# Performance work log

Measured on AMD Instinct MI355X. Metric: run time of the kernel, lower is better.

## Reference

```python
import jax, jax.numpy as jnp
import numpy as np
from jax.ops import segment_sum

N_GRAPHS, N_PER = 100, 1000
N = N_GRAPHS * N_PER
DEG = 32
E = N * DEG
RATIO = 0.8
K = int(np.ceil(RATIO * N_PER))  # 800, equal-size graphs -> fixed k
F_IN, F_MID, F_OUT = 128, 16, 256


def setup_inputs() -> dict:
    key = jax.random.key(0)
    ks = jax.random.split(key, 10)
    x = jax.random.normal(ks[0], (N, F_IN), dtype=jnp.float32)
    # intra-graph random edges
    epg = E // N_GRAPHS
    src_l = jax.random.randint(ks[1], (N_GRAPHS, epg), 0, N_PER)
    dst_l = jax.random.randint(ks[2], (N_GRAPHS, epg), 0, N_PER)
    offs = (jnp.arange(N_GRAPHS) * N_PER)[:, None]
    edge_index = jnp.stack([(src_l + offs).reshape(-1), (dst_l + offs).reshape(-1)]).astype(jnp.int32)
    batch = jnp.repeat(jnp.arange(N_GRAPHS, dtype=jnp.int32), N_PER)
    s = lambda fan: 1.0 / np.sqrt(fan)
    W1 = jax.random.normal(ks[3], (F_IN, F_MID), dtype=jnp.float32) * s(F_IN)
    b1 = jnp.zeros((F_MID,), dtype=jnp.float32)
    w_rel = jax.random.normal(ks[4], (F_MID, 1), dtype=jnp.float32) * s(F_MID)
    b_rel = jnp.zeros((1,), dtype=jnp.float32)
    w_root = jax.random.normal(ks[5], (F_MID, 1), dtype=jnp.float32) * s(F_MID)
    W2 = jax.random.normal(ks[6], (F_MID, F_OUT), dtype=jnp.float32) * s(F_MID)
    b2 = jnp.zeros((F_OUT,), dtype=jnp.float32)
    return {"x": x, "edge_index": edge_index, "batch": batch,
            "W1": W1, "b1": b1, "w_rel": w_rel, "b_rel": b_rel,
            "w_root": w_root, "W2": W2, "b2": b2}


def _gcn(x, src, dst, W, b, self_w, ew, n):
    # GCNConv with self-loops: D^{-1/2}(A+I)D^{-1/2} X W + b; masked variant
    deg = segment_sum(ew, dst, num_segments=n) + self_w
    dis = jnp.where(deg > 0, jax.lax.rsqrt(deg), 0.0)
    xw = x @ W
    coef = ew * dis[src] * dis[dst]                       # [E]
    agg = segment_sum(xw[src] * coef[:, None], dst, num_segments=n)
    agg = agg + xw * (self_w * dis * dis)[:, None]        # self-loop term
    return agg + b


def reference(x, edge_index, batch, W1, b1, w_rel, b_rel, w_root, W2, b2):
    src, dst = edge_index[0], edge_index[1]
    ones_n = jnp.ones((N,), dtype=x.dtype)
    ones_e = jnp.ones((src.shape[0],), dtype=x.dtype)
    # conv1 + relu
    h = jax.nn.relu(_gcn(x, src, dst, W1, b1, ones_n, ones_e, N))
    # SAGPooling score: GraphConv(16,1) -> tanh
    agg = segment_sum(h[src], dst, num_segments=N)
    score = jnp.tanh((agg @ w_rel + h @ w_root + b_rel)[:, 0])  # [N]
    # per-graph top-k (equal graph sizes -> fixed K), expressed as node mask
    sc2 = score.reshape(N_GRAPHS, N_PER)
    _, idx = jax.lax.top_k(sc2, K)
    mask = jnp.zeros((N_GRAPHS, N_PER), dtype=x.dtype)
    mask = mask.at[jnp.arange(N_GRAPHS)[:, None], idx].set(1.0).reshape(-1)  # [N]
    h = h * (score * mask)[:, None]                       # x[perm] * score[perm]
    em = mask[src] * mask[dst]                            # filter_adj as edge mask
    # conv2 + relu on surviving nodes only
    h2 = jax.nn.relu(_gcn(h, src, dst, W2, b2, mask, em, N)) * mask[:, None]
    # global mean pool over surviving nodes per graph
    sums = segment_sum(h2, batch, num_segments=N_GRAPHS)
    cnt = segment_sum(mask, batch, num_segments=N_GRAPHS)
    return sums / cnt[:, None]
```

## Files before the change

### kernel.cpp

```cpp
#include <hip/hip_runtime.h>
#include <math.h>

#define N_NODES 100000
#define NG 100
#define N_PER 1000
#define N_EDGES 3200000
#define EPG 32000
#define EPG4 8000
#define EPGP 35008
#define K_TOP 800
#define F_IN 128
#define F_MID 16
#define F_OUT 256
#define SENT 1000
#define NCH 8
#define CHN 128

typedef __attribute__((ext_vector_type(8))) short short8;
typedef __attribute__((ext_vector_type(4))) float floatx4;

__device__ __forceinline__ unsigned short f2bf(float x) {
    union { float f; unsigned int u; } c; c.f = x;
    unsigned int u = c.u;
    u = u + 0x7FFF + ((u >> 16) & 1);
    return (unsigned short)(u >> 16);
}
__device__ __forceinline__ void add4(float4& a, const float4 b) {
    a.x += b.x; a.y += b.y; a.z += b.z; a.w += b.w;
}
__device__ __forceinline__ unsigned int fkey(float f) {
    unsigned int u = __float_as_uint(f);
    return (u & 0x80000000u) ? ~u : (u | 0x80000000u);
}

__global__ __launch_bounds__(1024) void k_front(const float* __restrict__ x,
    const float* __restrict__ W1, const int* __restrict__ ei,
    unsigned short* __restrict__ csr, int* __restrict__ crG,
    float* __restrict__ dis1G, float* __restrict__ xw1)
{
    __shared__ int cnts[N_PER];
    __shared__ int rs[N_PER];
    __shared__ int scan[1024];
    __shared__ unsigned int rank4[EPG4];
    __shared__ __align__(16) unsigned short csrl[EPGP];

    int b = blockIdx.x, t = threadIdx.x;
    if (b < NG) {
        int g = b, ebase = g * EPG, nbase = g * N_PER;
        if (b == 0 && t < F_MID) xw1[(size_t)N_NODES * F_MID + t] = 0.f;
        const int4* dst4 = (const int4*)(ei + N_EDGES + ebase);
        const int4* src4 = (const int4*)(ei + ebase);
        if (t < N_PER) cnts[t] = 0;
        __syncthreads();
        for (int i = t; i < EPG4; i += 1024) {
            int4 d = dst4[i];
            unsigned r0 = (unsigned)atomicAdd(&cnts[d.x - nbase], 1);
            unsigned r1 = (unsigned)atomicAdd(&cnts[d.y - nbase], 1);
            unsigned r2 = (unsigned)atomicAdd(&cnts[d.z - nbase], 1);
            unsigned r3 = (unsigned)atomicAdd(&cnts[d.w - nbase], 1);
            rank4[i] = r0 | (r1 << 8) | (r2 << 16) | (r3 << 24);
        }
        __syncthreads();
        int c = (t < N_PER) ? cnts[t] : 0;
        int c4 = (c + 3) & ~3;
        scan[t] = c4;
        __syncthreads();
        for (int dd = 1; dd < 1024; dd <<= 1) {
            int v = (t >= dd) ? scan[t - dd] : 0;
            __syncthreads();
            scan[t] += v;
            __syncthreads();
        }
        int exc = scan[t] - c4;
        if (t < N_PER) {
            rs[t] = exc;
            crG[nbase + t] = (c << 16) | exc;
            dis1G[nbase + t] = rsqrtf((float)c + 1.0f);
            for (int q = c; q < c4; q++) csrl[exc + q] = (unsigned short)SENT;
        }
        __syncthreads();
        for (int i = t; i < EPG4; i += 1024) {
            int4 d = dst4[i];
            int4 s = src4[i];
            unsigned rk = rank4[i];
            csrl[rs[d.x - nbase] + (rk & 255u)]         = (unsigned short)(s.x - nbase);
            csrl[rs[d.y - nbase] + ((rk >> 8) & 255u)]  = (unsigned short)(s.y - nbase);
            csrl[rs[d.z - nbase] + ((rk >> 16) & 255u)] = (unsigned short)(s.z - nbase);
            csrl[rs[d.w - nbase] + (rk >> 24)]          = (unsigned short)(s.w - nbase);
        }
        __syncthreads();
        {
            const uint4* sv = (const uint4*)csrl;
            uint4* dv = (uint4*)(csr + (size_t)g * EPGP);
            for (int i = t; i < EPGP / 8; i += 1024) dv[i] = sv[i];
        }
    } else {
        int n = (b - NG) * 1024 + t;
        if (n >= N_NODES) return;
        const float4* xr = (const float4*)(x + (size_t)n * F_IN);
        float4 a0 = {0,0,0,0}, a1 = a0, a2 = a0, a3 = a0;
#pragma unroll 4
        for (int kk = 0; kk < 32; kk++) {
            float4 xv = xr[kk];
#pragma unroll
            for (int r = 0; r < 4; r++) {
                const float4* wr = (const float4*)(W1 + (kk * 4 + r) * F_MID);
                float xs = (r == 0) ? xv.x : (r == 1) ? xv.y : (r == 2) ? xv.z : xv.w;
                float4 w0 = wr[0], w1 = wr[1], w2 = wr[2], w3 = wr[3];
                a0.x = fmaf(xs, w0.x, a0.x); a0.y = fmaf(xs, w0.y, a0.y);
                a0.z = fmaf(xs, w0.z, a0.z); a0.w = fmaf(xs, w0.w, a0.w);
                a1.x = fmaf(xs, w1.x, a1.x); a1.y = fmaf(xs, w1.y, a1.y);
                a1.z = fmaf(xs, w1.z, a1.z); a1.w = fmaf(xs, w1.w, a1.w);
                a2.x = fmaf(xs, w2.x, a2.x); a2.y = fmaf(xs, w2.y, a2.y);
                a2.z = fmaf(xs, w2.z, a2.z); a2.w = fmaf(xs, w2.w, a2.w);
                a3.x = fmaf(xs, w3.x, a3.x); a3.y = fmaf(xs, w3.y, a3.y);
                a3.z = fmaf(xs, w3.z, a3.z); a3.w = fmaf(xs, w3.w, a3.w);
            }
        }
        float4* op = (float4*)(xw1 + (size_t)n * F_MID);
        op[0] = a0; op[1] = a1; op[2] = a2; op[3] = a3;
    }
}

__global__ __launch_bounds__(512) void k_conv1(const unsigned short* __restrict__ csr,
    const int* __restrict__ crG,
    const float* __restrict__ dis1G, const float* __restrict__ xw1,
    const float* __restrict__ b1, const float* __restrict__ w_rel,
    const float* __restrict__ w_root,
    float* __restrict__ hG, float* __restrict__ hwG, float* __restrict__ hroG)
{
    __shared__ float dis1l[N_PER + 1];
    int t = threadIdx.x, b = blockIdx.x;
    int g = b % NG, chunk = b / NG;
    int nbase = g * N_PER;
    const unsigned short* cg = csr + (size_t)g * EPGP;
    if (b == 0 && t < F_MID) hG[(size_t)N_NODES * F_MID + t] = 0.f;
    for (int i = t; i < N_PER; i += 512) dis1l[i] = dis1G[nbase + i];
    if (t == 0) dis1l[SENT] = 0.f;
    __syncthreads();

    int grp = t >> 2, l = t & 3;
    int n = chunk * CHN + grp;
    if (n >= N_PER) return;
    int cr = crG[nbase + n];
    int c4 = ((cr >> 16) + 3) & ~3;
    const unsigned short* cp = cg + (cr & 0xFFFF);
    float4 a0 = {0,0,0,0}, a1 = a0, a2 = a0, a3 = a0;
    for (int k = 0; k < c4; k += 4) {
        uint2 wv = *(const uint2*)(cp + k);
        int s0 = wv.x & 0xFFFF, s1 = wv.x >> 16, s2 = wv.y & 0xFFFF, s3 = wv.y >> 16;
        float4 v0 = *(const float4*)(xw1 + ((size_t)(nbase + s0) << 4) + 4 * l);
        float4 v1 = *(const float4*)(xw1 + ((size_t)(nbase + s1) << 4) + 4 * l);
        float4 v2 = *(const float4*)(xw1 + ((size_t)(nbase + s2) << 4) + 4 * l);
        float4 v3 = *(const float4*)(xw1 + ((size_t)(nbase + s3) << 4) + 4 * l);
        float w0 = dis1l[s0], w1 = dis1l[s1], w2 = dis1l[s2], w3 = dis1l[s3];
        a0.x = fmaf(v0.x, w0, a0.x); a0.y = fmaf(v0.y, w0, a0.y); a0.z = fmaf(v0.z, w0, a0.z); a0.w = fmaf(v0.w, w0, a0.w);
        a1.x = fmaf(v1.x, w1, a1.x); a1.y = fmaf(v1.y, w1, a1.y); a1.z = fmaf(v1.z, w1, a1.z); a1.w = fmaf(v1.w, w1, a1.w);
        a2.x = fmaf(v2.x, w2, a2.x); a2.y = fmaf(v2.y, w2, a2.y); a2.z = fmaf(v2.z, w2, a2.z); a2.w = fmaf(v2.w, w2, a2.w);
        a3.x = fmaf(v3.x, w3, a3.x); a3.y = fmaf(v3.y, w3, a3.y); a3.z = fmaf(v3.z, w3, a3.z); a3.w = fmaf(v3.w, w3, a3.w);
    }
    add4(a0, a1); add4(a2, a3); add4(a0, a2);
    float dn = dis1l[n];
    float4 sfr = *(const float4*)(xw1 + ((size_t)(nbase + n) << 4) + 4 * l);
    float4 b14 = *(const float4*)(b1 + 4 * l);
    float4 hv;
    hv.x = fmaxf(fmaf(dn, fmaf(sfr.x, dn, a0.x), b14.x), 0.f);
    hv.y = fmaxf(fmaf(dn, fmaf(sfr.y, dn, a0.y), b14.y), 0.f);
    hv.z = fmaxf(fmaf(dn, fmaf(sfr.z, dn, a0.z), b14.z), 0.f);
    hv.w = fmaxf(fmaf(dn, fmaf(sfr.w, dn, a0.w), b14.w), 0.f);
    *(float4*)(hG + ((size_t)(nbase + n) << 4) + 4 * l) = hv;

    float4 wr4 = *(const float4*)(w_rel + 4 * l);
    float4 wo4 = *(const float4*)(w_root + 4 * l);
    float p1 = hv.x * wr4.x + hv.y * wr4.y + hv.z * wr4.z + hv.w * wr4.w;
    float p2 = hv.x * wo4.x + hv.y * wo4.y + hv.z * wo4.z + hv.w * wo4.w;
    p1 += __shfl_xor(p1, 1); p1 += __shfl_xor(p1, 2);
    p2 += __shfl_xor(p2, 1); p2 += __shfl_xor(p2, 2);
    if (l == 0) { hwG[nbase + n] = p1; hroG[nbase + n] = p2; }
}

__global__ __launch_bounds__(1024) void k_mid(const unsigned short* __restrict__ csr,
    const int* __restrict__ crG,
    const float* __restrict__ hwG, const float* __restrict__ hroG,
    const float* __restrict__ b_rel,
    float* __restrict__ mskG, float* __restrict__ dis2G, float* __restrict__ wsrcG,
    float* __restrict__ out)
{
    __shared__ float hwl[N_PER + 1];
    __shared__ float sc[N_PER];
    __shared__ float msk[N_PER + 1];
    __shared__ int cntl[N_PER];
    __shared__ int rsl[N_PER];
    __shared__ int hist[1024];
    __shared__ int sh_b1, sh_r1, sh_b2, sh_r2, sh_len, sh_cntgt;
    __shared__ float sh_thr;

    int t = threadIdx.x, g = blockIdx.x;
    int nbase = g * N_PER;
    const unsigned short* cg = csr + (size_t)g * EPGP;
    int grp = t >> 2, l = t & 3;

    if (t < N_PER) {
        int cr = crG[nbase + t];
        cntl[t] = cr >> 16; rsl[t] = cr & 0xFFFF;
        hwl[t] = hwG[nbase + t];
    }
    if (t == 0) { sh_cntgt = 0; sh_len = 0; hwl[SENT] = 0.f; }
    if (t < F_OUT) out[g * F_OUT + t] = 0.f;
    float brel = b_rel[0];
    __syncthreads();

#pragma unroll
    for (int rr = 0; rr < 4; rr++) {
        int n = grp + 256 * rr;
        if (n < N_PER) {
            int c4 = (cntl[n] + 3) & ~3;
            const unsigned short* cp = cg + rsl[n];
            float sm = 0.f;
            for (int k = 0; k < c4; k += 4) {
                uint2 wv = *(const uint2*)(cp + k);
                int s = (l == 0) ? (int)(wv.x & 0xFFFF) : (l == 1) ? (int)(wv.x >> 16)
                      : (l == 2) ? (int)(wv.y & 0xFFFF) : (int)(wv.y >> 16);
                sm += hwl[s];
            }
            sm += __shfl_xor(sm, 1); sm += __shfl_xor(sm, 2);
            if (l == 0) sc[n] = tanhf(sm + hroG[nbase + n] + brel);
        }
    }
    __syncthreads();

    unsigned int mykey = (t < N_PER) ? fkey(sc[t]) : 0u;
    hist[t] = 0;
    __syncthreads();
    if (t < N_PER) atomicAdd(&hist[mykey >> 22], 1);
    __syncthreads();
    {
        int v0 = hist[t]; __syncthreads();
        hist[1023 - t] = v0; __syncthreads();
        for (int dd = 1; dd < 1024; dd <<= 1) {
            int v = (t >= dd) ? hist[t - dd] : 0;
            __syncthreads(); hist[t] += v; __syncthreads();
        }
        int Sb = hist[1023 - t];
        int Snext = (t == 1023) ? 0 : hist[1022 - t];
        if (Sb >= K_TOP && Snext < K_TOP) { sh_b1 = t; sh_r1 = K_TOP - Snext; }
    }
    __syncthreads();
    int b1v = sh_b1, r1 = sh_r1;
    hist[t] = 0;
    __syncthreads();
    if (t < N_PER && (int)(mykey >> 22) == b1v) atomicAdd(&hist[(mykey >> 12) & 1023], 1);
    __syncthreads();
    {
        int v0 = hist[t]; __syncthreads();
        hist[1023 - t] = v0; __syncthreads();
        for (int dd = 1; dd < 1024; dd <<= 1) {
            int v = (t >= dd) ? hist[t - dd] : 0;
            __syncthreads(); hist[t] += v; __syncthreads();
        }
        int Sb = hist[1023 - t];
        int Snext = (t == 1023) ? 0 : hist[1022 - t];
        if (Sb >= r1 && Snext < r1) { sh_b2 = t; sh_r2 = r1 - Snext; }
    }
    __syncthreads();
    unsigned int pref = ((unsigned int)b1v << 10) | (unsigned int)sh_b2;
    int r2 = sh_r2;
    __syncthreads();
    if (t < N_PER && (mykey >> 12) == pref) { int p = atomicAdd(&sh_len, 1); hist[p] = (int)mykey; }
    __syncthreads();
    {
        int L = sh_len;
        if (t < L) {
            unsigned int k0 = (unsigned int)hist[t];
            int gcnt = 0, ecnt = 0;
            for (int q2 = 0; q2 < L; q2++) {
                unsigned int kq = (unsigned int)hist[q2];
                gcnt += (kq > k0); ecnt += (kq == k0);
            }
            if (gcnt < r2 && r2 <= gcnt + ecnt)
                sh_thr = __uint_as_float((k0 & 0x80000000u) ? (k0 & 0x7FFFFFFFu) : ~k0);
        }
    }
    __syncthreads();
    float thr = sh_thr;

    {
        bool pred = (t < N_PER) && (sc[t] > thr);
        unsigned long long bal = __ballot(pred);
        if ((t & 63) == 0) atomicAdd(&sh_cntgt, (int)__popcll(bal));
    }
    __syncthreads();
    {
        int need = K_TOP - sh_cntgt;
        if (t < N_PER) {
            float v = sc[t];
            float mm;
            if (v > thr) mm = 1.f;
            else if (v < thr) mm = 0.f;
            else {
                int r = 0;
                for (int q2 = 0; q2 < t; q2++) if (sc[q2] == thr) r++;
                mm = (r < need) ? 1.f : 0.f;
            }
            msk[t] = mm;
        }
        if (t == 0) msk[SENT] = 0.f;
    }
    __syncthreads();

#pragma unroll
    for (int rr = 0; rr < 4; rr++) {
        int n = grp + 256 * rr;
        if (n < N_PER) {
            int c4 = (cntl[n] + 3) & ~3;
            const unsigned short* cp = cg + rsl[n];
            float sm = 0.f;
            for (int k = 0; k < c4; k += 4) {
                uint2 wv = *(const uint2*)(cp + k);
                int s = (l == 0) ? (int)(wv.x & 0xFFFF) : (l == 1) ? (int)(wv.x >> 16)
                      : (l == 2) ? (int)(wv.y & 0xFFFF) : (int)(wv.y >> 16);
                sm += msk[s];
            }
            sm += __shfl_xor(sm, 1); sm += __shfl_xor(sm, 2);
            if (l == 0) {
                float d2 = msk[n] * (sm + 1.f);
                float di = (d2 > 0.f) ? rsqrtf(d2) : 0.f;
                mskG[nbase + n] = msk[n];
                dis2G[nbase + n] = di;
                wsrcG[nbase + n] = sc[n] * msk[n] * di;
            }
        }
    }
}

__global__ __launch_bounds__(512) void k_conv2(const unsigned short* __restrict__ csr,
    const int* __restrict__ crG,
    const float* __restrict__ hG, const float* __restrict__ wsrcG,
    const float* __restrict__ dis2G, const float* __restrict__ mskG,
    const float* __restrict__ W2, const float* __restrict__ b2,
    float* __restrict__ out)
{
    __shared__ float wsrcl[N_PER + 1];
    __shared__ __align__(16) unsigned short fbf[CHN * F_MID];
    __shared__ __align__(16) unsigned short w2t[F_OUT * F_MID];
    __shared__ float mskl[CHN];
    int t = threadIdx.x, b = blockIdx.x;
    int g = b % NG, chunk = b / NG;
    int nbase = g * N_PER, n0 = chunk * CHN;
    const unsigned short* cg = csr + (size_t)g * EPGP;

    for (int i = t; i < N_PER; i += 512) wsrcl[i] = wsrcG[nbase + i];
    if (t == 0) wsrcl[SENT] = 0.f;
    for (int i = t; i < F_OUT * F_MID; i += 512) {
        int f = i >> 4, jj = i & 15;
        w2t[i] = f2bf(W2[jj * F_OUT + f]);
    }
    __syncthreads();

    int grp = t >> 2, l = t & 3;
    int n = n0 + grp;
    if (n < N_PER) {
        float di = dis2G[nbase + n];
        float4 pv = {0.f, 0.f, 0.f, 0.f};
        if (di != 0.f) {
            int cr = crG[nbase + n];
            int c4 = ((cr >> 16) + 3) & ~3;
            const unsigned short* cp = cg + (cr & 0xFFFF);
            float4 a0 = {0,0,0,0}, a1 = a0, a2 = a0, a3 = a0;
            for (int k = 0; k < c4; k += 4) {
                uint2 wv = *(const uint2*)(cp + k);
                int s0 = wv.x & 0xFFFF, s1 = wv.x >> 16, s2 = wv.y & 0xFFFF, s3 = wv.y >> 16;
                float4 v0 = *(const float4*)(hG + ((size_t)(nbase + s0) << 4) + 4 * l);
                float4 v1 = *(const float4*)(hG + ((size_t)(nbase + s1) << 4) + 4 * l);
                float4 v2 = *(const float4*)(hG + ((size_t)(nbase + s2) << 4) + 4 * l);
                float4 v3 = *(const float4*)(hG + ((size_t)(nbase + s3) << 4) + 4 * l);
                float w0 = wsrcl[s0], w1 = wsrcl[s1], w2 = wsrcl[s2], w3 = wsrcl[s3];
                a0.x = fmaf(v0.x, w0, a0.x); a0.y = fmaf(v0.y, w0, a0.y); a0.z = fmaf(v0.z, w0, a0.z); a0.w = fmaf(v0.w, w0, a0.w);
                a1.x = fmaf(v1.x, w1, a1.x); a1.y = fmaf(v1.y, w1, a1.y); a1.z = fmaf(v1.z, w1, a1.z); a1.w = fmaf(v1.w, w1, a1.w);
                a2.x = fmaf(v2.x, w2, a2.x); a2.y = fmaf(v2.y, w2, a2.y); a2.z = fmaf(v2.z, w2, a2.z); a2.w = fmaf(v2.w, w2, a2.w);
                a3.x = fmaf(v3.x, w3, a3.x); a3.y = fmaf(v3.y, w3, a3.y); a3.z = fmaf(v3.z, w3, a3.z); a3.w = fmaf(v3.w, w3, a3.w);
            }
            add4(a0, a1); add4(a2, a3); add4(a0, a2);
            float wn = wsrcl[n];
            float4 hs = *(const float4*)(hG + ((size_t)(nbase + n) << 4) + 4 * l);
            pv.x = di * fmaf(hs.x, wn, a0.x);
            pv.y = di * fmaf(hs.y, wn, a0.y);
            pv.z = di * fmaf(hs.z, wn, a0.z);
            pv.w = di * fmaf(hs.w, wn, a0.w);
        }
        unsigned int pk0 = (unsigned int)f2bf(pv.x) | ((unsigned int)f2bf(pv.y) << 16);
        unsigned int pk1 = (unsigned int)f2bf(pv.z) | ((unsigned int)f2bf(pv.w) << 16);
        *(unsigned int*)(fbf + grp * F_MID + 4 * l) = pk0;
        *(unsigned int*)(fbf + grp * F_MID + 4 * l + 2) = pk1;
        if (l == 0) mskl[grp] = mskG[nbase + n];
    } else {
        *(unsigned int*)(fbf + grp * F_MID + 4 * l) = 0u;
        *(unsigned int*)(fbf + grp * F_MID + 4 * l + 2) = 0u;
        if (l == 0) mskl[grp] = 0.f;
    }
    __syncthreads();

    {
        int wave = t >> 6, lane = t & 63;
        int q = lane >> 4, fl = lane & 15;
        int c0 = 32 * wave + fl, c1 = c0 + 16;
        float b2f0 = b2[c0], b2f1 = b2[c1];
        short8 bfrag0 = {0,0,0,0,0,0,0,0}, bfrag1 = bfrag0;
        if (q < 2) {
            bfrag0 = *(const short8*)(w2t + c0 * F_MID + q * 8);
            bfrag1 = *(const short8*)(w2t + c1 * F_MID + q * 8);
        }
        floatx4 zero = {0.f, 0.f, 0.f, 0.f};
        float acc0 = 0.f, acc1 = 0.f;
        for (int tile = 0; tile < CHN / 16; tile++) {
            short8 afrag = {0,0,0,0,0,0,0,0};
            int na = tile * 16 + fl;
            if (q < 2)
                afrag = *(const short8*)(fbf + na * F_MID + q * 8);
            floatx4 d0 = __builtin_amdgcn_mfma_f32_16x16x32_bf16(afrag, bfrag0, zero, 0, 0, 0);
            floatx4 d1 = __builtin_amdgcn_mfma_f32_16x16x32_bf16(afrag, bfrag1, zero, 0, 0, 0);
#pragma unroll
            for (int r = 0; r < 4; r++) {
                int nd = tile * 16 + q * 4 + r;
                float m = mskl[nd];
                acc0 += m * fmaxf(d0[r] + b2f0, 0.f);
                acc1 += m * fmaxf(d1[r] + b2f1, 0.f);
            }
        }
        acc0 += __shfl_xor(acc0, 16); acc0 += __shfl_xor(acc0, 32);
        acc1 += __shfl_xor(acc1, 16); acc1 += __shfl_xor(acc1, 32);
        if (lane < 16) {
            atomicAdd(&out[g * F_OUT + c0], acc0 * (1.0f / (float)K_TOP));
            atomicAdd(&out[g * F_OUT + c1], acc1 * (1.0f / (float)K_TOP));
        }
    }
}

extern "C" void kernel_launch(void* const* d_in, const int* in_sizes, int n_in,
                              void* d_out, int out_size, void* d_ws, size_t ws_size,
                              hipStream_t stream) {
    const float* x      = (const float*)d_in[0];
    const int*   ei     = (const int*)d_in[1];
    const float* W1     = (const float*)d_in[3];
    const float* b1     = (const float*)d_in[4];
    const float* w_rel  = (const float*)d_in[5];
    const float* b_rel  = (const float*)d_in[6];
    const float* w_root = (const float*)d_in[7];
    const float* W2     = (const float*)d_in[8];
    const float* b2     = (const float*)d_in[9];
    float* out = (float*)d_out;

    char* ws = (char*)d_ws;
    size_t o = 0;
    auto nxt = [&](size_t bytes) { void* p = ws + o; o += (bytes + 255) & ~(size_t)255; return p; };
    unsigned short* csr = (unsigned short*)nxt((size_t)NG * EPGP * sizeof(unsigned short));
    int*   crG   = (int*)nxt((size_t)N_NODES * sizeof(int));
    float* dis1G = (float*)nxt((size_t)N_NODES * sizeof(float));
    float* xw1   = (float*)nxt(((size_t)N_NODES + 1) * F_MID * sizeof(float));
    float* hG    = (float*)nxt(((size_t)N_NODES + 1) * F_MID * sizeof(float));
    float* hwG   = (float*)nxt((size_t)N_NODES * sizeof(float));
    float* hroG  = (float*)nxt((size_t)N_NODES * sizeof(float));
    float* mskG  = (float*)nxt((size_t)N_NODES * sizeof(float));
    float* dis2G = (float*)nxt((size_t)N_NODES * sizeof(float));
    float* wsrcG = (float*)nxt((size_t)N_NODES * sizeof(float));

    int gemm_blocks = (N_NODES + 1023) / 1024;
    k_front<<<NG + gemm_blocks, 1024, 0, stream>>>(x, W1, ei, csr, crG, dis1G, xw1);
    k_conv1<<<NG * NCH, 512, 0, stream>>>(csr, crG, dis1G, xw1, b1, w_rel, w_root, hG, hwG, hroG);
    k_mid<<<NG, 1024, 0, stream>>>(csr, crG, hwG, hroG, b_rel, mskG, dis2G, wsrcG, out);
    k_conv2<<<NG * NCH, 512, 0, stream>>>(csr, crG, hG, wsrcG, dis2G, mskG, W2, b2, out);
}
```

Before: 224.7 us.

## Stage pre-scaled per-graph features in LDS for conv gathers

Both GCN aggregation kernels now copy the whole graph's feature rows into shared memory, pre-multiplied by the per-source normalisation weight. The neighbour gathers then become plain adds from swizzled LDS instead of scattered global loads plus multiplies. The swizzle is meant to reduce bank conflicts. In exchange, each block loads the full graph even though it only processes one chunk of nodes, and the large LDS footprint may cut occupancy. The global sentinel-row zeroing is also dropped.

```diff
diff --git a/kernel.cpp b/kernel.cpp
--- a/kernel.cpp
+++ b/kernel.cpp
@@ -27,6 +27,9 @@
 }
 __device__ __forceinline__ void add4(float4& a, const float4 b) {
     a.x += b.x; a.y += b.y; a.z += b.z; a.w += b.w;
+}
+__device__ __forceinline__ int fidx4(int s, int l) {
+    return s * 16 + ((4 * (l + ((s >> 1) & 3))) & 15);
 }
 __device__ __forceinline__ unsigned int fkey(float f) {
     unsigned int u = __float_as_uint(f);
@@ -129,14 +132,22 @@
     const float* __restrict__ w_root,
     float* __restrict__ hG, float* __restrict__ hwG, float* __restrict__ hroG)
 {
-    __shared__ float dis1l[N_PER + 1];
+    __shared__ __align__(16) float feat[(N_PER + 1) * F_MID];
     int t = threadIdx.x, b = blockIdx.x;
     int g = b % NG, chunk = b / NG;
     int nbase = g * N_PER;
     const unsigned short* cg = csr + (size_t)g * EPGP;
-    if (b == 0 && t < F_MID) hG[(size_t)N_NODES * F_MID + t] = 0.f;
-    for (int i = t; i < N_PER; i += 512) dis1l[i] = dis1G[nbase + i];
-    if (t == 0) dis1l[SENT] = 0.f;
+    {
+        const float4* xsrc = (const float4*)(xw1 + (size_t)nbase * F_MID);
+        for (int i = t; i < N_PER * 4; i += 512) {
+            int nn = i >> 2, q = i & 3;
+            float4 v = xsrc[i];
+            float d = dis1G[nbase + nn];
+            v.x *= d; v.y *= d; v.z *= d; v.w *= d;
+            *(float4*)(feat + fidx4(nn, q)) = v;
+        }
+        if (t < 4) { float4 z = {0.f, 0.f, 0.f, 0.f}; *(float4*)(feat + fidx4(SENT, t)) = z; }
+    }
     __syncthreads();
 
     int grp = t >> 2, l = t & 3;
@@ -149,25 +160,20 @@
     for (int k = 0; k < c4; k += 4) {
         uint2 wv = *(const uint2*)(cp + k);
         int s0 = wv.x & 0xFFFF, s1 = wv.x >> 16, s2 = wv.y & 0xFFFF, s3 = wv.y >> 16;
-        float4 v0 = *(const float4*)(xw1 + ((size_t)(nbase + s0) << 4) + 4 * l);
-        float4 v1 = *(const float4*)(xw1 + ((size_t)(nbase + s1) << 4) + 4 * l);
-        float4 v2 = *(const float4*)(xw1 + ((size_t)(nbase + s2) << 4) + 4 * l);
-        float4 v3 = *(const float4*)(xw1 + ((size_t)(nbase + s3) << 4) + 4 * l);
-        float w0 = dis1l[s0], w1 = dis1l[s1], w2 = dis1l[s2], w3 = dis1l[s3];
-        a0.x = fmaf(v0.x, w0, a0.x); a0.y = fmaf(v0.y, w0, a0.y); a0.z = fmaf(v0.z, w0, a0.z); a0.w = fmaf(v0.w, w0, a0.w);
-        a1.x = fmaf(v1.x, w1, a1.x); a1.y = fmaf(v1.y, w1, a1.y); a1.z = fmaf(v1.z, w1, a1.z); a1.w = fmaf(v1.w, w1, a1.w);
-        a2.x = fmaf(v2.x, w2, a2.x); a2.y = fmaf(v2.y, w2, a2.y); a2.z = fmaf(v2.z, w2, a2.z); a2.w = fmaf(v2.w, w2, a2.w);
-        a3.x = fmaf(v3.x, w3, a3.x); a3.y = fmaf(v3.y, w3, a3.y); a3.z = fmaf(v3.z, w3, a3.z); a3.w = fmaf(v3.w, w3, a3.w);
+        add4(a0, *(const float4*)(feat + fidx4(s0, l)));
+        add4(a1, *(const float4*)(feat + fidx4(s1, l)));
+        add4(a2, *(const float4*)(feat + fidx4(s2, l)));
+        add4(a3, *(const float4*)(feat + fidx4(s3, l)));
     }
     add4(a0, a1); add4(a2, a3); add4(a0, a2);
-    float dn = dis1l[n];
-    float4 sfr = *(const float4*)(xw1 + ((size_t)(nbase + n) << 4) + 4 * l);
+    float dn = dis1G[nbase + n];
+    float4 sf = *(const float4*)(feat + fidx4(n, l));
     float4 b14 = *(const float4*)(b1 + 4 * l);
     float4 hv;
-    hv.x = fmaxf(fmaf(dn, fmaf(sfr.x, dn, a0.x), b14.x), 0.f);
-    hv.y = fmaxf(fmaf(dn, fmaf(sfr.y, dn, a0.y), b14.y), 0.f);
-    hv.z = fmaxf(fmaf(dn, fmaf(sfr.z, dn, a0.z), b14.z), 0.f);
-    hv.w = fmaxf(fmaf(dn, fmaf(sfr.w, dn, a0.w), b14.w), 0.f);
+    hv.x = fmaxf(fmaf(dn, a0.x + sf.x, b14.x), 0.f);
+    hv.y = fmaxf(fmaf(dn, a0.y + sf.y, b14.y), 0.f);
+    hv.z = fmaxf(fmaf(dn, a0.z + sf.z, b14.z), 0.f);
+    hv.w = fmaxf(fmaf(dn, a0.w + sf.w, b14.w), 0.f);
     *(float4*)(hG + ((size_t)(nbase + n) << 4) + 4 * l) = hv;
 
     float4 wr4 = *(const float4*)(w_rel + 4 * l);
@@ -340,7 +346,7 @@
     const float* __restrict__ W2, const float* __restrict__ b2,
     float* __restrict__ out)
 {
-    __shared__ float wsrcl[N_PER + 1];
+    __shared__ __align__(16) float feat2[(N_PER + 1) * F_MID];
     __shared__ __align__(16) unsigned short fbf[CHN * F_MID];
     __shared__ __align__(16) unsigned short w2t[F_OUT * F_MID];
     __shared__ float mskl[CHN];
@@ -349,8 +355,17 @@
     int nbase = g * N_PER, n0 = chunk * CHN;
     const unsigned short* cg = csr + (size_t)g * EPGP;
 
-    for (int i = t; i < N_PER; i += 512) wsrcl[i] = wsrcG[nbase + i];
-    if (t == 0) wsrcl[SENT] = 0.f;
+    {
+        const float4* hsrc = (const float4*)(hG + (size_t)nbase * F_MID);
+        for (int i = t; i < N_PER * 4; i += 512) {
+            int nn = i >> 2, q = i & 3;
+            float4 v = hsrc[i];
+            float w = wsrcG[nbase + nn];
+            v.x *= w; v.y *= w; v.z *= w; v.w *= w;
+            *(float4*)(feat2 + fidx4(nn, q)) = v;
+        }
+        if (t < 4) { float4 z = {0.f, 0.f, 0.f, 0.f}; *(float4*)(feat2 + fidx4(SENT, t)) = z; }
+    }
     for (int i = t; i < F_OUT * F_MID; i += 512) {
         int f = i >> 4, jj = i & 15;
         w2t[i] = f2bf(W2[jj * F_OUT + f]);
@@ -370,23 +385,17 @@
             for (int k = 0; k < c4; k += 4) {
                 uint2 wv = *(const uint2*)(cp + k);
                 int s0 = wv.x & 0xFFFF, s1 = wv.x >> 16, s2 = wv.y & 0xFFFF, s3 = wv.y >> 16;
-                float4 v0 = *(const float4*)(hG + ((size_t)(nbase + s0) << 4) + 4 * l);
-                float4 v1 = *(const float4*)(hG + ((size_t)(nbase + s1) << 4) + 4 * l);
-                float4 v2 = *(const float4*)(hG + ((size_t)(nbase + s2) << 4) + 4 * l);
-                float4 v3 = *(const float4*)(hG + ((size_t)(nbase + s3) << 4) + 4 * l);
-                float w0 = wsrcl[s0], w1 = wsrcl[s1], w2 = wsrcl[s2], w3 = wsrcl[s3];
-                a0.x = fmaf(v0.x, w0, a0.x); a0.y = fmaf(v0.y, w0, a0.y); a0.z = fmaf(v0.z, w0, a0.z); a0.w = fmaf(v0.w, w0, a0.w);
-                a1.x = fmaf(v1.x, w1, a1.x); a1.y = fmaf(v1.y, w1, a1.y); a1.z = fmaf(v1.z, w1, a1.z); a1.w = fmaf(v1.w, w1, a1.w);
-                a2.x = fmaf(v2.x, w2, a2.x); a2.y = fmaf(v2.y, w2, a2.y); a2.z = fmaf(v2.z, w2, a2.z); a2.w = fmaf(v2.w, w2, a2.w);
-                a3.x = fmaf(v3.x, w3, a3.x); a3.y = fmaf(v3.y, w3, a3.y); a3.z = fmaf(v3.z, w3, a3.z); a3.w = fmaf(v3.w, w3, a3.w);
+                add4(a0, *(const float4*)(feat2 + fidx4(s0, l)));
+                add4(a1, *(const float4*)(feat2 + fidx4(s1, l)));
+                add4(a2, *(const float4*)(feat2 + fidx4(s2, l)));
+                add4(a3, *(const float4*)(feat2 + fidx4(s3, l)));
             }
             add4(a0, a1); add4(a2, a3); add4(a0, a2);
-            float wn = wsrcl[n];
-            float4 hs = *(const float4*)(hG + ((size_t)(nbase + n) << 4) + 4 * l);
-            pv.x = di * fmaf(hs.x, wn, a0.x);
-            pv.y = di * fmaf(hs.y, wn, a0.y);
-            pv.z = di * fmaf(hs.z, wn, a0.z);
-            pv.w = di * fmaf(hs.w, wn, a0.w);
+            float4 sf = *(const float4*)(feat2 + fidx4(n, l));
+            pv.x = di * (a0.x + sf.x);
+            pv.y = di * (a0.y + sf.y);
+            pv.z = di * (a0.z + sf.z);
+            pv.w = di * (a0.w + sf.w);
         }
         unsigned int pk0 = (unsigned int)f2bf(pv.x) | ((unsigned int)f2bf(pv.y) << 16);
         unsigned int pk1 = (unsigned int)f2bf(pv.z) | ((unsigned int)f2bf(pv.w) << 16);
```

After: 212.4 us, median of 2. 5.5% less time.
